# Kernel optimization log

Hardware: AMD Instinct MI355X
Metric: run time of the kernel (lower is better)

Reference implementation:

```python
import jax, jax.numpy as jnp
import numpy as np

D, NQ, BS, NL, NH, NP, DFF = 256, 900, 8, 4, 8, 4, 1024
HD = D // NH
SHAPES = np.array([[100, 100], [50, 50], [25, 25], [13, 13]], dtype=np.int64)  # (H, W) per level
LSTART = np.concatenate([[0], np.cumsum(SHAPES[:, 0] * SHAPES[:, 1])[:-1]]).astype(np.int64)
LMEM = int((SHAPES[:, 0] * SHAPES[:, 1]).sum())


def layer_norm(x, g, b, eps=1e-5):
    mu = x.mean(-1, keepdims=True)
    var = ((x - mu) ** 2).mean(-1, keepdims=True)
    return (x - mu) * jax.lax.rsqrt(var + eps) * g + b


def _forward(tgt, tgt_query_pos, tgt_reference_points, memory,
             in_proj_w, in_proj_b, out_proj_w, out_proj_b,
             samp_off_w, samp_off_b, attn_w_w, attn_w_b,
             value_proj_w, value_proj_b, output_proj_w, output_proj_b,
             lin1_w, lin1_b, lin2_w, lin2_b,
             norm1_g, norm1_b, norm2_g, norm2_b, norm3_g, norm3_b):
    # ---- self-attention (seq-first, torch nn.MultiheadAttention semantics) ----
    q = tgt + tgt_query_pos  # q = k = with_pos_embed(tgt, pos)
    Wq, Wk, Wv = jnp.split(in_proj_w, 3, 0)
    bq, bk, bv = jnp.split(in_proj_b, 3, 0)
    def heads(x):  # (nq, bs, d) -> (bs, nh, nq, hd)
        return x.reshape(NQ, BS, NH, HD).transpose(1, 2, 0, 3)
    qh = heads(q @ Wq.T + bq)
    kh = heads(q @ Wk.T + bk)
    vh = heads(tgt @ Wv.T + bv)
    attn = jax.nn.softmax(jnp.einsum('bhqd,bhkd->bhqk', qh, kh) / np.float32(np.sqrt(HD)), -1)
    sa = jnp.einsum('bhqk,bhkd->bhqd', attn, vh).transpose(2, 0, 1, 3).reshape(NQ, BS, D)
    sa = sa @ out_proj_w.T + out_proj_b
    t = layer_norm(tgt + sa, norm2_g, norm2_b)

    # ---- MSDeformAttn cross-attention (batch-first internally) ----
    qb = (t + tgt_query_pos).transpose(1, 0, 2)          # (bs, nq, d)
    refb = tgt_reference_points.transpose(1, 0, 2, 3)    # (bs, nq, nl, 2) in [0,1]
    memb = memory.transpose(1, 0, 2)                     # (bs, L, d)
    value = (memb @ value_proj_w.T + value_proj_b).reshape(BS, LMEM, NH, HD)
    off = (qb @ samp_off_w.T + samp_off_b).reshape(BS, NQ, NH, NL, NP, 2)
    aw = jax.nn.softmax((qb @ attn_w_w.T + attn_w_b).reshape(BS, NQ, NH, NL * NP), -1)
    aw = aw.reshape(BS, NQ, NH, NL, NP)
    normz = jnp.asarray(SHAPES[:, ::-1].copy(), dtype=jnp.float32)  # (nl, 2) = [W, H]
    loc = refb[:, :, None, :, None, :] + off / normz[None, None, None, :, None, :]

    out = jnp.zeros((BS, NQ, NH, HD), jnp.float32)
    for l in range(NL):  # fixed small number of pyramid levels
        Hl, Wl = int(SHAPES[l, 0]), int(SHAPES[l, 1])
        s = int(LSTART[l])
        v_l = value[:, s:s + Hl * Wl]  # (bs, Hl*Wl, nh, hd)
        # grid_sample(align_corners=False, padding=zeros) pixel coords
        x = (loc[:, :, :, l, :, 0] * Wl - 0.5).transpose(0, 1, 3, 2).reshape(BS, NQ * NP, NH)
        y = (loc[:, :, :, l, :, 1] * Hl - 0.5).transpose(0, 1, 3, 2).reshape(BS, NQ * NP, NH)
        x0 = jnp.floor(x)
        y0 = jnp.floor(y)
        samp = jnp.zeros((BS, NQ * NP, NH, HD), jnp.float32)
        for dx in (0, 1):
            for dy in (0, 1):
                xc = x0 + dx
                yc = y0 + dy
                w = (1.0 - jnp.abs(x - xc)) * (1.0 - jnp.abs(y - yc))
                valid = (xc >= 0) & (xc < Wl) & (yc >= 0) & (yc < Hl)
                idx = (jnp.clip(yc, 0, Hl - 1) * Wl + jnp.clip(xc, 0, Wl - 1)).astype(jnp.int32)
                g = jnp.take_along_axis(v_l, idx[..., None], axis=1)  # (bs, nq*np, nh, hd)
                samp = samp + jnp.where(valid, w, 0.0)[..., None] * g
        samp = samp.reshape(BS, NQ, NP, NH, HD)
        out = out + jnp.einsum('bqhp,bqphd->bqhd', aw[:, :, :, l], samp)
    ca = (out.reshape(BS, NQ, D) @ output_proj_w.T + output_proj_b).transpose(1, 0, 2)
    t = layer_norm(t + ca, norm1_g, norm1_b)

    # ---- FFN ----
    ffn = jax.nn.relu(t @ lin1_w.T + lin1_b) @ lin2_w.T + lin2_b
    return layer_norm(t + ffn, norm3_g, norm3_b)


def setup_inputs() -> dict:
    key = jax.random.key(0)
    ks = jax.random.split(key, 24)
    r = lambda i, shape, s: jax.random.normal(ks[i], shape, jnp.float32) * s
    return {
        'tgt': r(0, (NQ, BS, D), 1.0),
        'tgt_query_pos': r(1, (NQ, BS, D), 1.0),
        'tgt_reference_points': jax.random.uniform(ks[2], (NQ, BS, NL, 2), jnp.float32),
        'memory': r(3, (LMEM, BS, D), 1.0),
        'spatial_shapes': jnp.asarray(SHAPES),
        'level_start_index': jnp.asarray(LSTART),
        'in_proj_w': r(4, (3 * D, D), 0.02), 'in_proj_b': r(5, (3 * D,), 0.02),
        'out_proj_w': r(6, (D, D), 0.02), 'out_proj_b': r(7, (D,), 0.02),
        'samp_off_w': r(8, (NH * NL * NP * 2, D), 0.01), 'samp_off_b': r(9, (NH * NL * NP * 2,), 0.01),
        'attn_w_w': r(10, (NH * NL * NP, D), 0.02), 'attn_w_b': r(11, (NH * NL * NP,), 0.02),
        'value_proj_w': r(12, (D, D), 0.02), 'value_proj_b': r(13, (D,), 0.02),
        'output_proj_w': r(14, (D, D), 0.02), 'output_proj_b': r(15, (D,), 0.02),
        'lin1_w': r(16, (DFF, D), 0.02), 'lin1_b': r(17, (DFF,), 0.02),
        'lin2_w': r(18, (D, DFF), 0.02), 'lin2_b': r(19, (D,), 0.02),
        'norm1_g': jnp.ones((D,), jnp.float32), 'norm1_b': jnp.zeros((D,), jnp.float32),
        'norm2_g': jnp.ones((D,), jnp.float32), 'norm2_b': jnp.zeros((D,), jnp.float32),
        'norm3_g': jnp.ones((D,), jnp.float32), 'norm3_b': jnp.zeros((D,), jnp.float32),
    }


def reference(tgt, tgt_query_pos, tgt_reference_points, memory, spatial_shapes, level_start_index,
              in_proj_w, in_proj_b, out_proj_w, out_proj_b, samp_off_w, samp_off_b,
              attn_w_w, attn_w_b, value_proj_w, value_proj_b, output_proj_w, output_proj_b,
              lin1_w, lin1_b, lin2_w, lin2_b, norm1_g, norm1_b, norm2_g, norm2_b, norm3_g, norm3_b):
    # spatial_shapes / level_start_index are static level constants (module-level SHAPES/LSTART)
    return _forward(tgt, tgt_query_pos, tgt_reference_points, memory,
                    in_proj_w, in_proj_b, out_proj_w, out_proj_b,
                    samp_off_w, samp_off_b, attn_w_w, attn_w_b,
                    value_proj_w, value_proj_b, output_proj_w, output_proj_b,
                    lin1_w, lin1_b, lin2_w, lin2_b,
                    norm1_g, norm1_b, norm2_g, norm2_b, norm3_g, norm3_b)
```

## Files before the change

kernel.cpp:

```cpp
#include <hip/hip_runtime.h>
#include <hip/hip_bf16.h>


namespace {
constexpr int D_ = 256;
constexpr int NQ_ = 900;
constexpr int BS_ = 8;
constexpr int NH_ = 8;
constexpr int HD_ = 32;
constexpr int DFF_ = 1024;
constexpr int MTOK = NQ_ * BS_;
constexpr int LMEM_ = 13294;
constexpr long T = (long)MTOK * D_;
constexpr float QSC = 0.17677669529663687f;
constexpr int QKVS = 768;
constexpr int MVAL = BS_ * LMEM_;
}

typedef __attribute__((ext_vector_type(8))) short bf8_t;
typedef __attribute__((ext_vector_type(4))) float f4_t;

#define MFMA16(a, b, c) __builtin_amdgcn_mfma_f32_16x16x32_bf16((a), (b), (c), 0, 0, 0)

__device__ __forceinline__ unsigned short bfbits(float x) {
    union { __hip_bfloat16 h; unsigned short u; } cv;
    cv.h = __float2bfloat16(x);
    return cv.u;
}
__device__ __forceinline__ float bf2f(unsigned short u) {
    union { float f; unsigned v; } cv;
    cv.v = ((unsigned)u) << 16;
    return cv.f;
}

__device__ __forceinline__ void gload16(const unsigned short* g, unsigned short* l) {
    __builtin_amdgcn_global_load_lds(
        (const __attribute__((address_space(1))) unsigned int*)(g),
        (__attribute__((address_space(3))) unsigned int*)(l), 16, 0, 0);
}
__device__ __forceinline__ void gload16f(const float* g, float* l) {
    __builtin_amdgcn_global_load_lds(
        (const __attribute__((address_space(1))) unsigned int*)(g),
        (__attribute__((address_space(3))) unsigned int*)(l), 16, 0, 0);
}

__global__ void conv_weights(
    const float* __restrict__ ipw, const float* __restrict__ opw,
    const float* __restrict__ sow, const float* __restrict__ aww,
    const float* __restrict__ vpw, const float* __restrict__ outpw,
    const float* __restrict__ l1w, const float* __restrict__ l2w,
    const float* __restrict__ ipb, const float* __restrict__ sob,
    const float* __restrict__ awb,
    unsigned short* __restrict__ Wbf, float* __restrict__ biasAll)
{
    if (blockIdx.x == 0) {
        for (int j = threadIdx.x; j < 768; j += 256)
            biasAll[j] = (j < 256) ? ipb[j] * QSC : ipb[j];
        for (int j = threadIdx.x; j < 384; j += 256)
            biasAll[768 + j] = (j < 256) ? sob[j] : awb[j - 256];
    }
    const long idx4 = (long)blockIdx.x * 256 + threadIdx.x;
    if (idx4 >= 253952) return;
    const long e = idx4 * 4;
    const float* src; long off; float sc = 1.f;
    if (e < 196608)      { src = ipw;   off = 0;      if (e < 65536) sc = QSC; }
    else if (e < 262144) { src = opw;   off = 196608; }
    else if (e < 327680) { src = sow;   off = 262144; }
    else if (e < 360448) { src = aww;   off = 327680; }
    else if (e < 425984) { src = vpw;   off = 360448; }
    else if (e < 491520) { src = outpw; off = 425984; }
    else if (e < 753664) { src = l1w;   off = 491520; }
    else                 { src = l2w;   off = 753664; }
    const float4 v = *(const float4*)(src + (e - off));
    union { unsigned short u[4]; uint2 w; } pk;
    pk.u[0] = bfbits(v.x * sc); pk.u[1] = bfbits(v.y * sc);
    pk.u[2] = bfbits(v.z * sc); pk.u[3] = bfbits(v.w * sc);
    *(uint2*)(Wbf + e) = pk.w;
}

template<bool RELU, bool OUTBF16>
__global__ __launch_bounds__(256) void gemm_mfma(
    const unsigned short* __restrict__ A, const unsigned short* __restrict__ W,
    const float* __restrict__ bias, void* __restrict__ C, int M, int N, int K)
{
    __shared__ unsigned short As[128 * 32];
    __shared__ unsigned short Ws[128 * 32];
    const int t = threadIdx.x;
    const long m0 = (long)blockIdx.x * 128;
    const int n0 = blockIdx.y * 128;
    const int row0 = t >> 2;
    const int cgp = (t & 3) ^ ((t >> 2) & 3);
    long ar0 = m0 + row0;        if (ar0 > M - 1) ar0 = M - 1;
    long ar1 = m0 + 64 + row0;   if (ar1 > M - 1) ar1 = M - 1;
    const unsigned short* ga0 = A + ar0 * K + cgp * 8;
    const unsigned short* ga1 = A + ar1 * K + cgp * 8;
    const unsigned short* gw0 = W + (long)(n0 + row0) * K + cgp * 8;
    const unsigned short* gw1 = W + (long)(n0 + 64 + row0) * K + cgp * 8;
    const int lane = t & 63, wave = t >> 6;
    const int c = lane & 15, g = lane >> 4;
    const int wr = wave >> 1, wc = wave & 1;
    const int sws = (g * 8) ^ ((c & 3) * 8);
    f4_t acc[4][4];
#pragma unroll
    for (int i = 0; i < 4; ++i)
#pragma unroll
        for (int j = 0; j < 4; ++j)
            acc[i][j] = f4_t{0.f, 0.f, 0.f, 0.f};

    for (int kb = 0; kb < K; kb += 32) {
        gload16(ga0 + kb, As + t * 8);
        gload16(ga1 + kb, As + 2048 + t * 8);
        gload16(gw0 + kb, Ws + t * 8);
        gload16(gw1 + kb, Ws + 2048 + t * 8);
        __syncthreads();
        bf8_t af[4], bfr[4];
#pragma unroll
        for (int i = 0; i < 4; ++i) {
            af[i] = *(const bf8_t*)(As + (wr * 64 + i * 16 + c) * 32 + sws);
            bfr[i] = *(const bf8_t*)(Ws + (wc * 64 + i * 16 + c) * 32 + sws);
        }
#pragma unroll
        for (int i = 0; i < 4; ++i)
#pragma unroll
            for (int j = 0; j < 4; ++j)
                acc[i][j] = MFMA16(af[i], bfr[j], acc[i][j]);
        __syncthreads();
    }

#pragma unroll
    for (int i = 0; i < 4; ++i) {
        const long rbase = m0 + wr * 64 + i * 16 + 4 * g;
#pragma unroll
        for (int j = 0; j < 4; ++j) {
            const int col = n0 + wc * 64 + j * 16 + c;
            const float bv = bias[col];
#pragma unroll
            for (int r = 0; r < 4; ++r) {
                const long rr = rbase + r;
                if (rr < M) {
                    float v = acc[i][j][r] + bv;
                    if (RELU) v = fmaxf(v, 0.f);
                    if (OUTBF16) ((unsigned short*)C)[rr * N + col] = bfbits(v);
                    else         ((float*)C)[rr * N + col] = v;
                }
            }
        }
    }
}

__global__ __launch_bounds__(256) void gemm_f32d(
    const float* __restrict__ A, const unsigned short* __restrict__ W,
    const float* __restrict__ bias, unsigned short* __restrict__ C,
    int M, int N, int K)
{
    __shared__ float Asf[64 * 64];
    __shared__ unsigned short Ws[128 * 64];
    const int t = threadIdx.x;
    const long m0 = (long)blockIdx.x * 64;
    const int n0 = blockIdx.y * 128;
    const float* gA[4];
#pragma unroll
    for (int l = 0; l < 4; ++l) {
        int r = (int)m0 + l * 16 + (t >> 4); if (r > M - 1) r = M - 1;
        const int sp = (t & 15) ^ ((t >> 4) & 15);
        gA[l] = A + (long)r * K + sp * 4;
    }
    const unsigned short* gW[4];
#pragma unroll
    for (int l = 0; l < 4; ++l) {
        const int r = l * 32 + (t >> 3);
        const int sp = (t & 7) ^ (r & 7);
        gW[l] = W + (long)(n0 + r) * K + sp * 8;
    }
    const int lane = t & 63, wave = t >> 6;
    const int c = lane & 15, g = lane >> 4;
    const int wr = wave >> 1, wc = wave & 1;
    f4_t acc[2][4];
#pragma unroll
    for (int i = 0; i < 2; ++i)
#pragma unroll
        for (int j = 0; j < 4; ++j)
            acc[i][j] = f4_t{0.f, 0.f, 0.f, 0.f};

    for (int kb = 0; kb < K; kb += 64) {
#pragma unroll
        for (int l = 0; l < 4; ++l) gload16f(gA[l] + kb, Asf + l * 1024 + t * 4);
#pragma unroll
        for (int l = 0; l < 4; ++l) gload16(gW[l] + kb, Ws + l * 2048 + t * 8);
        __syncthreads();
#pragma unroll
        for (int s = 0; s < 2; ++s) {
            bf8_t af[2], bfr[4];
#pragma unroll
            for (int i = 0; i < 2; ++i) {
                const int row = wr * 32 + i * 16 + c;
                const int sl0 = (s * 8 + 2 * g) ^ (row & 15);
                const int sl1 = (s * 8 + 2 * g + 1) ^ (row & 15);
                const f4_t lo = *(const f4_t*)(Asf + row * 64 + sl0 * 4);
                const f4_t hi = *(const f4_t*)(Asf + row * 64 + sl1 * 4);
                union { bf8_t v; unsigned short u[8]; } pk;
                pk.u[0] = bfbits(lo[0]); pk.u[1] = bfbits(lo[1]);
                pk.u[2] = bfbits(lo[2]); pk.u[3] = bfbits(lo[3]);
                pk.u[4] = bfbits(hi[0]); pk.u[5] = bfbits(hi[1]);
                pk.u[6] = bfbits(hi[2]); pk.u[7] = bfbits(hi[3]);
                af[i] = pk.v;
            }
#pragma unroll
            for (int j = 0; j < 4; ++j) {
                const int row = wc * 64 + j * 16 + c;
                const int sl = (s * 4 + g) ^ (row & 7);
                bfr[j] = *(const bf8_t*)(Ws + row * 64 + sl * 8);
            }
#pragma unroll
            for (int i = 0; i < 2; ++i)
#pragma unroll
                for (int j = 0; j < 4; ++j)
                    acc[i][j] = MFMA16(af[i], bfr[j], acc[i][j]);
        }
        __syncthreads();
    }

    unsigned short* Cl = (unsigned short*)Asf;
#pragma unroll
    for (int i = 0; i < 2; ++i) {
        const int rloc = wr * 32 + i * 16 + 4 * g;
#pragma unroll
        for (int j = 0; j < 4; ++j) {
            const int col = wc * 64 + j * 16 + c;
            const float bv = bias[n0 + col];
#pragma unroll
            for (int r = 0; r < 4; ++r)
                Cl[(rloc + r) * 128 + col] = bfbits(acc[i][j][r] + bv);
        }
    }
    __syncthreads();
    {
        const int row = t >> 2, seg = t & 3;
        const long rr = m0 + row;
        if (rr < M) {
            const uint4* src = (const uint4*)(Cl + row * 128 + seg * 32);
            uint4* dst = (uint4*)(C + rr * N + n0 + seg * 32);
            dst[0] = src[0]; dst[1] = src[1]; dst[2] = src[2]; dst[3] = src[3];
        }
    }
}

template<bool OUTBF16>
__global__ __launch_bounds__(256) void gemm_f32a(
    const float* __restrict__ A, const float* __restrict__ A2,
    const unsigned short* __restrict__ W, const float* __restrict__ bias,
    void* __restrict__ C, int M, int N, int K, int addLim)
{
    __shared__ unsigned short As[128 * 32];
    __shared__ unsigned short Ws[128 * 32];
    const int t = threadIdx.x;
    const long m0 = (long)blockIdx.x * 128;
    const int n0 = blockIdx.y * 128;
    const bool useAdd = n0 < addLim;
    const int row0 = t >> 2, cg = t & 3;
    const int cgp = cg ^ ((t >> 2) & 3);
    long ar0 = m0 + row0;        if (ar0 > M - 1) ar0 = M - 1;
    long ar1 = m0 + 64 + row0;   if (ar1 > M - 1) ar1 = M - 1;
    const float* Ap0 = A + ar0 * K + cg * 8;
    const float* Ap1 = A + ar1 * K + cg * 8;
    const float* Bp0 = A2 + ar0 * K + cg * 8;
    const float* Bp1 = A2 + ar1 * K + cg * 8;
    const unsigned short* gw0 = W + (long)(n0 + row0) * K + cgp * 8;
    const unsigned short* gw1 = W + (long)(n0 + 64 + row0) * K + cgp * 8;
    unsigned short* la0 = As + row0 * 32 + ((cg * 8) ^ ((row0 & 3) * 8));
    unsigned short* la1 = la0 + 2048;
    const int lane = t & 63, wave = t >> 6;
    const int c = lane & 15, g = lane >> 4;
    const int wr = wave >> 1, wc = wave & 1;
    const int sws = (g * 8) ^ ((c & 3) * 8);
    f4_t acc[4][4];
#pragma unroll
    for (int i = 0; i < 4; ++i)
#pragma unroll
        for (int j = 0; j < 4; ++j)
            acc[i][j] = f4_t{0.f, 0.f, 0.f, 0.f};

    for (int kb = 0; kb < K; kb += 32) {
        gload16(gw0 + kb, Ws + t * 8);
        gload16(gw1 + kb, Ws + 2048 + t * 8);
        float4 a00 = *(const float4*)(Ap0 + kb);
        float4 a01 = *(const float4*)(Ap0 + kb + 4);
        float4 a10 = *(const float4*)(Ap1 + kb);
        float4 a11 = *(const float4*)(Ap1 + kb + 4);
        if (useAdd) {
            const float4 b00 = *(const float4*)(Bp0 + kb);
            const float4 b01 = *(const float4*)(Bp0 + kb + 4);
            const float4 b10 = *(const float4*)(Bp1 + kb);
            const float4 b11 = *(const float4*)(Bp1 + kb + 4);
            a00.x += b00.x; a00.y += b00.y; a00.z += b00.z; a00.w += b00.w;
            a01.x += b01.x; a01.y += b01.y; a01.z += b01.z; a01.w += b01.w;
            a10.x += b10.x; a10.y += b10.y; a10.z += b10.z; a10.w += b10.w;
            a11.x += b11.x; a11.y += b11.y; a11.z += b11.z; a11.w += b11.w;
        }
        union { bf8_t v; unsigned short u[8]; } p0, p1;
        p0.u[0] = bfbits(a00.x); p0.u[1] = bfbits(a00.y); p0.u[2] = bfbits(a00.z); p0.u[3] = bfbits(a00.w);
        p0.u[4] = bfbits(a01.x); p0.u[5] = bfbits(a01.y); p0.u[6] = bfbits(a01.z); p0.u[7] = bfbits(a01.w);
        p1.u[0] = bfbits(a10.x); p1.u[1] = bfbits(a10.y); p1.u[2] = bfbits(a10.z); p1.u[3] = bfbits(a10.w);
        p1.u[4] = bfbits(a11.x); p1.u[5] = bfbits(a11.y); p1.u[6] = bfbits(a11.z); p1.u[7] = bfbits(a11.w);
        *(bf8_t*)la0 = p0.v;
        *(bf8_t*)la1 = p1.v;
        __syncthreads();
        bf8_t af[4], bfr[4];
#pragma unroll
        for (int i = 0; i < 4; ++i) {
            af[i] = *(const bf8_t*)(As + (wr * 64 + i * 16 + c) * 32 + sws);
            bfr[i] = *(const bf8_t*)(Ws + (wc * 64 + i * 16 + c) * 32 + sws);
        }
#pragma unroll
        for (int i = 0; i < 4; ++i)
#pragma unroll
            for (int j = 0; j < 4; ++j)
                acc[i][j] = MFMA16(af[i], bfr[j], acc[i][j]);
        __syncthreads();
    }

#pragma unroll
    for (int i = 0; i < 4; ++i) {
        const long rbase = m0 + wr * 64 + i * 16 + 4 * g;
#pragma unroll
        for (int j = 0; j < 4; ++j) {
            const int col = n0 + wc * 64 + j * 16 + c;
            const float bv = bias[col];
#pragma unroll
            for (int r = 0; r < 4; ++r) {
                const long rr = rbase + r;
                if (rr < M) {
                    float v = acc[i][j][r] + bv;
                    if (OUTBF16) ((unsigned short*)C)[rr * N + col] = bfbits(v);
                    else         ((float*)C)[rr * N + col] = v;
                }
            }
        }
    }
}

__global__ __launch_bounds__(256) void attn_mfma(
    const unsigned short* __restrict__ Qb, const unsigned short* __restrict__ Kb,
    const unsigned short* __restrict__ Vb, unsigned short* __restrict__ sa)
{
    __shared__ float smemf[2112];
    unsigned short* Ks = (unsigned short*)smemf;
    unsigned short* Vt = (unsigned short*)(smemf + 1024);
    const int t = threadIdx.x;
    const int wave = t >> 6, lane = t & 63;
    const int g = lane >> 4, c = lane & 15;
    const int b = blockIdx.x >> 3, h = blockIdx.x & 7;
    const int q0 = blockIdx.y * 64 + wave * 16;
    const int q = q0 + c;
    const bool qv = q < NQ_;
    const bf8_t qf = *(const bf8_t*)(Qb + ((long)(qv ? q : 0) * BS_ + b) * QKVS + h * HD_ + 8 * g);

    f4_t acc0 = {0.f, 0.f, 0.f, 0.f}, acc1 = {0.f, 0.f, 0.f, 0.f};
    float m_run = -1e30f, l_run = 0.f;
    const int sk = t >> 2, sd = (t & 3) * 8;

    for (int kc = 0; kc < NQ_; kc += 64) {
        __syncthreads();
        {
            const int key = kc + sk;
            union { bf8_t v; unsigned short u[8]; } kv, vv;
            if (key < NQ_) {
                kv.v = *(const bf8_t*)(Kb + ((long)key * BS_ + b) * QKVS + h * HD_ + sd);
                vv.v = *(const bf8_t*)(Vb + ((long)key * BS_ + b) * QKVS + h * HD_ + sd);
            } else {
#pragma unroll
                for (int u = 0; u < 8; ++u) { kv.u[u] = 0; vv.u[u] = 0; }
            }
            *(bf8_t*)(Ks + sk * 32 + sd) = kv.v;
#pragma unroll
            for (int u = 0; u < 8; ++u) {
                const int r = sd + u;
                Vt[r * 64 + (sk ^ ((r & 7) << 3))] = vv.u[u];
            }
        }
        __syncthreads();

        f4_t s[4];
#pragma unroll
        for (int tt = 0; tt < 4; ++tt) {
            const bf8_t kf = *(const bf8_t*)(Ks + (tt * 16 + c) * 32 + 8 * g);
            f4_t z = {0.f, 0.f, 0.f, 0.f};
            s[tt] = MFMA16(kf, qf, z);
        }
        float sv[16];
#pragma unroll
        for (int tt = 0; tt < 4; ++tt)
#pragma unroll
            for (int r = 0; r < 4; ++r) {
                float x = s[tt][r];
                if (kc + tt * 16 + 4 * g + r >= NQ_) x = -1e30f;
                sv[tt * 4 + r] = x;
            }
        float mloc = sv[0];
#pragma unroll
        for (int i = 1; i < 16; ++i) mloc = fmaxf(mloc, sv[i]);
        mloc = fmaxf(mloc, __shfl_xor(mloc, 16));
        mloc = fmaxf(mloc, __shfl_xor(mloc, 32));
        const float mnew = fmaxf(m_run, mloc);
        const float resc = __expf(m_run - mnew);
        float p[16], ls = 0.f;
#pragma unroll
        for (int i = 0; i < 16; ++i) { p[i] = __expf(sv[i] - mnew); ls += p[i]; }
        ls += __shfl_xor(ls, 16);
        ls += __shfl_xor(ls, 32);
        l_run = l_run * resc + ls;
        m_run = mnew;
#pragma unroll
        for (int r = 0; r < 4; ++r) { acc0[r] *= resc; acc1[r] *= resc; }

        unsigned pk[4][2];
#pragma unroll
        for (int tt = 0; tt < 4; ++tt) {
            pk[tt][0] = (unsigned)bfbits(p[tt * 4 + 0]) | ((unsigned)bfbits(p[tt * 4 + 1]) << 16);
            pk[tt][1] = (unsigned)bfbits(p[tt * 4 + 2]) | ((unsigned)bfbits(p[tt * 4 + 3]) << 16);
        }
        const int srcA = ((g & 1) << 5) + c;
        const int srcB = srcA + 16;
#pragma unroll
        for (int kh = 0; kh < 2; ++kh) {
            const unsigned a0 = __shfl(pk[kh * 2][0], srcA), b0_ = __shfl(pk[kh * 2 + 1][0], srcA);
            const unsigned a1 = __shfl(pk[kh * 2][1], srcA), b1_ = __shfl(pk[kh * 2 + 1][1], srcA);
            const unsigned a2 = __shfl(pk[kh * 2][0], srcB), b2_ = __shfl(pk[kh * 2 + 1][0], srcB);
            const unsigned a3 = __shfl(pk[kh * 2][1], srcB), b3_ = __shfl(pk[kh * 2 + 1][1], srcB);
            union { bf8_t v; unsigned u[4]; } pf;
            const bool hi = (g & 2);
            pf.u[0] = hi ? b0_ : a0; pf.u[1] = hi ? b1_ : a1;
            pf.u[2] = hi ? b2_ : a2; pf.u[3] = hi ? b3_ : a3;
            const int kcol = (kh * 32 + 8 * g) ^ ((c & 7) << 3);
            const bf8_t vf0 = *(const bf8_t*)(Vt + c * 64 + kcol);
            const bf8_t vf1 = *(const bf8_t*)(Vt + (16 + c) * 64 + kcol);
            acc0 = MFMA16(vf0, pf.v, acc0);
            acc1 = MFMA16(vf1, pf.v, acc1);
        }
    }

    __syncthreads();
    const float invl = 1.f / l_run;
    float* O = smemf + wave * 528;
#pragma unroll
    for (int r = 0; r < 4; ++r) {
        O[c * 33 + 4 * g + r] = acc0[r] * invl;
        O[c * 33 + 16 + 4 * g + r] = acc1[r] * invl;
    }
    __syncthreads();
    {
        const int ql = lane >> 2, part = lane & 3;
        const int qg = q0 + ql;
        if (qg < NQ_) {
            union { bf8_t v; unsigned short u[8]; } pk;
#pragma unroll
            for (int u = 0; u < 8; ++u) pk.u[u] = bfbits(O[ql * 33 + part * 8 + u]);
            *(bf8_t*)(sa + ((long)qg * BS_ + b) * D_ + h * HD_ + part * 8) = pk.v;
        }
    }
}

__global__ __launch_bounds__(256) void msdeform_kernel(
    const float* __restrict__ oa, const float* __restrict__ refp,
    const unsigned short* __restrict__ val, unsigned short* __restrict__ out)
{
    __shared__ float saw[128];
    __shared__ float redm[8], redi[8];
    __shared__ float swt[128][4];
    __shared__ int sidx[128][4];
    const int bq = blockIdx.x;
    const int b = bq / NQ_, q = bq % NQ_;
    const int t = threadIdx.x;
    if (t < 128) saw[t] = oa[(long)bq * 384 + 256 + t];
    __syncthreads();
    if (t < 8) {
        float mx = -1e30f;
        for (int i = 0; i < 16; ++i) mx = fmaxf(mx, saw[t * 16 + i]);
        float s = 0.f;
        for (int i = 0; i < 16; ++i) s += __expf(saw[t * 16 + i] - mx);
        redm[t] = mx; redi[t] = 1.f / s;
    }
    __syncthreads();
    if (t < 128) {
        const int h = t >> 4, lp = t & 15, l = lp >> 2, p = lp & 3;
        const float aw = __expf(saw[t] - redm[h]) * redi[h];
        const int Wi = (l == 0) ? 100 : (l == 1) ? 50 : (l == 2) ? 25 : 13;
        const int Hi = Wi;
        const int sl = (l == 0) ? 0 : (l == 1) ? 10000 : (l == 2) ? 12500 : 13125;
        const float offx = oa[(long)bq * 384 + h * 32 + l * 8 + p * 2 + 0];
        const float offy = oa[(long)bq * 384 + h * 32 + l * 8 + p * 2 + 1];
        const float refx = refp[(((long)q * BS_ + b) * 4 + l) * 2 + 0];
        const float refy = refp[(((long)q * BS_ + b) * 4 + l) * 2 + 1];
        const float fW = (float)Wi, fH = (float)Hi;
        const float x = (refx + offx / fW) * fW - 0.5f;
        const float y = (refy + offy / fH) * fH - 0.5f;
        const float x0f = floorf(x), y0f = floorf(y);
        const float fx = x - x0f, fy = y - y0f;
        const int ix = (int)x0f, iy = (int)y0f;
        const float wts[4] = {(1.f - fx) * (1.f - fy), fx * (1.f - fy),
                              (1.f - fx) * fy,          fx * fy};
        const int xs[4] = {ix, ix + 1, ix, ix + 1};
        const int ys[4] = {iy, iy, iy + 1, iy + 1};
#pragma unroll
        for (int tap = 0; tap < 4; ++tap) {
            const bool valid = (xs[tap] >= 0) & (xs[tap] < Wi) & (ys[tap] >= 0) & (ys[tap] < Hi);
            const int xc = min(max(xs[tap], 0), Wi - 1);
            const int yc = min(max(ys[tap], 0), Hi - 1);
            swt[t][tap] = valid ? aw * wts[tap] : 0.f;
            sidx[t][tap] = ((sl + yc * Wi + xc) << 3) + b;
        }
    }
    __syncthreads();
    const int h = t >> 5, r = t & 31, qd = r & 7, s = r >> 3;
    float a0 = 0.f, a1 = 0.f, a2 = 0.f, a3 = 0.f;
#pragma unroll
    for (int i = 0; i < 16; ++i) {
        const int j = h * 16 + i;
        const float wv = swt[j][s];
        const long base = (long)sidx[j][s] * D_ + h * HD_ + qd * 4;
        const uint2 raw = *(const uint2*)(val + base);
        a0 += wv * bf2f((unsigned short)(raw.x & 0xffff));
        a1 += wv * bf2f((unsigned short)(raw.x >> 16));
        a2 += wv * bf2f((unsigned short)(raw.y & 0xffff));
        a3 += wv * bf2f((unsigned short)(raw.y >> 16));
    }
    a0 += __shfl_xor(a0, 8); a0 += __shfl_xor(a0, 16);
    a1 += __shfl_xor(a1, 8); a1 += __shfl_xor(a1, 16);
    a2 += __shfl_xor(a2, 8); a2 += __shfl_xor(a2, 16);
    a3 += __shfl_xor(a3, 8); a3 += __shfl_xor(a3, 16);
    if (s == 0) {
        union { unsigned short u[4]; uint2 w; } pk;
        pk.u[0] = bfbits(a0); pk.u[1] = bfbits(a1); pk.u[2] = bfbits(a2); pk.u[3] = bfbits(a3);
        *(uint2*)(out + (long)bq * D_ + h * HD_ + qd * 4) = pk.w;
    }
}

__global__ __launch_bounds__(256) void ln_kernel(
    const float* __restrict__ inA, const float* __restrict__ inB,
    const float* __restrict__ g, const float* __restrict__ be,
    float* __restrict__ out, const float* __restrict__ pos,
    unsigned short* __restrict__ bfOut, int swapB, int bfMode)
{
    const int r = blockIdx.x * 4 + (threadIdx.x >> 6);
    const int lane = threadIdx.x & 63;
    long rb = r;
    if (swapB) rb = (long)(r & 7) * NQ_ + (r >> 3);
    const float4 a4 = *(const float4*)(inA + (long)r * D_ + lane * 4);
    const float4 b4 = *(const float4*)(inB + rb * D_ + lane * 4);
    float x[4] = {a4.x + b4.x, a4.y + b4.y, a4.z + b4.z, a4.w + b4.w};
    float s = x[0] + x[1] + x[2] + x[3];
#pragma unroll
    for (int off = 32; off > 0; off >>= 1) s += __shfl_xor(s, off);
    const float mu = s * (1.f / D_);
    float v = 0.f;
#pragma unroll
    for (int cc = 0; cc < 4; ++cc) { const float dd = x[cc] - mu; v += dd * dd; }
#pragma unroll
    for (int off = 32; off > 0; off >>= 1) v += __shfl_xor(v, off);
    const float rs = rsqrtf(v * (1.f / D_) + 1e-5f);
    const float4 g4 = *(const float4*)(g + lane * 4);
    const float4 e4 = *(const float4*)(be + lane * 4);
    const float gg[4] = {g4.x, g4.y, g4.z, g4.w};
    const float ee[4] = {e4.x, e4.y, e4.z, e4.w};
    float y[4];
#pragma unroll
    for (int cc = 0; cc < 4; ++cc) y[cc] = (x[cc] - mu) * rs * gg[cc] + ee[cc];
    *(float4*)(out + (long)r * D_ + lane * 4) = make_float4(y[0], y[1], y[2], y[3]);
    if (bfMode) {
        float z[4] = {y[0], y[1], y[2], y[3]};
        long er = r;
        if (bfMode == 2) {
            const float4 p4 = *(const float4*)(pos + (long)r * D_ + lane * 4);
            z[0] += p4.x; z[1] += p4.y; z[2] += p4.z; z[3] += p4.w;
            er = (long)(r & 7) * NQ_ + (r >> 3);
        }
        union { unsigned short u[4]; uint2 w; } pk;
        pk.u[0] = bfbits(z[0]); pk.u[1] = bfbits(z[1]);
        pk.u[2] = bfbits(z[2]); pk.u[3] = bfbits(z[3]);
        *(uint2*)(bfOut + er * D_ + lane * 4) = pk.w;
    }
}

extern "C" void kernel_launch(void* const* d_in, const int* in_sizes, int n_in,
                              void* d_out, int out_size, void* d_ws, size_t ws_size,
                              hipStream_t stream) {
    const float* tgt   = (const float*)d_in[0];
    const float* pos   = (const float*)d_in[1];
    const float* refp  = (const float*)d_in[2];
    const float* mem   = (const float*)d_in[3];
    const float* ipw   = (const float*)d_in[6];
    const float* ipb   = (const float*)d_in[7];
    const float* opw   = (const float*)d_in[8];
    const float* opb   = (const float*)d_in[9];
    const float* sow   = (const float*)d_in[10];
    const float* sob   = (const float*)d_in[11];
    const float* aww   = (const float*)d_in[12];
    const float* awb   = (const float*)d_in[13];
    const float* vpw   = (const float*)d_in[14];
    const float* vpb   = (const float*)d_in[15];
    const float* outpw = (const float*)d_in[16];
    const float* outpb = (const float*)d_in[17];
    const float* l1w   = (const float*)d_in[18];
    const float* l1b   = (const float*)d_in[19];
    const float* l2w   = (const float*)d_in[20];
    const float* l2b   = (const float*)d_in[21];
    const float* n1g = (const float*)d_in[22]; const float* n1be = (const float*)d_in[23];
    const float* n2g = (const float*)d_in[24]; const float* n2be = (const float*)d_in[25];
    const float* n3g = (const float*)d_in[26]; const float* n3be = (const float*)d_in[27];

    char* wsb = (char*)d_ws;
    auto alloc = [&](size_t bytes) { char* p = wsb; wsb += (bytes + 255) & ~(size_t)255; return p; };
    unsigned short* Wbf       = (unsigned short*)alloc(1015808 * 2);
    float*          biasAll   = (float*)alloc(1152 * 4);
    unsigned short* QKV_bf    = (unsigned short*)alloc((long)MTOK * QKVS * 2);
    unsigned short* sa_bf     = (unsigned short*)alloc(T * 2);
    float*          saproj    = (float*)alloc(T * 4);
    float*          t1        = (float*)alloc(T * 4);
    unsigned short* qplus2_bf = (unsigned short*)alloc(T * 2);
    float*          oa        = (float*)alloc((long)MTOK * 384 * 4);
    unsigned short* sampo_bf  = (unsigned short*)alloc(T * 2);
    float*          ca        = (float*)alloc(T * 4);
    float*          t2        = (float*)alloc(T * 4);
    unsigned short* t2_bf     = (unsigned short*)alloc(T * 2);
    unsigned short* ffnh_bf   = (unsigned short*)alloc((long)MTOK * DFF_ * 2);
    float*          ffno      = (float*)alloc(T * 4);
    unsigned short* val       = (unsigned short*)alloc((long)MVAL * D_ * 2);
    const unsigned short* wqkv  = Wbf + 0;
    const unsigned short* wo    = Wbf + 196608;
    const unsigned short* wsoaw = Wbf + 262144;
    const unsigned short* wvp   = Wbf + 360448;
    const unsigned short* wop   = Wbf + 425984;
    const unsigned short* wl1   = Wbf + 491520;
    const unsigned short* wl2   = Wbf + 753664;
    const float* bias_qkv = biasAll;
    const float* bias_oa  = biasAll + 768;

    const dim3 blk(256);
    const dim3 g_m(57, 2);

    conv_weights<<<992, blk, 0, stream>>>(ipw, opw, sow, aww, vpw, outpw, l1w, l2w,
                                          ipb, sob, awb, Wbf, biasAll);
    gemm_f32a<true><<<dim3(57, 6), blk, 0, stream>>>(tgt, pos, wqkv, bias_qkv, QKV_bf,
                                                     MTOK, QKVS, D_, 512);
    attn_mfma<<<dim3(64, 15), blk, 0, stream>>>(QKV_bf, QKV_bf + 256, QKV_bf + 512, sa_bf);
    gemm_mfma<false, false><<<g_m, blk, 0, stream>>>(sa_bf, wo, opb, saproj, MTOK, D_, D_);
    ln_kernel<<<1800, blk, 0, stream>>>(tgt, saproj, n2g, n2be, t1, pos, qplus2_bf, 0, 2);
    gemm_f32d<<<dim3(1662, 2), blk, 0, stream>>>(mem, wvp, vpb, val, MVAL, D_, D_);
    gemm_mfma<false, false><<<dim3(57, 3), blk, 0, stream>>>(qplus2_bf, wsoaw, bias_oa, oa, MTOK, 384, D_);
    msdeform_kernel<<<7200, blk, 0, stream>>>(oa, refp, val, sampo_bf);
    gemm_mfma<false, false><<<g_m, blk, 0, stream>>>(sampo_bf, wop, outpb, ca, MTOK, D_, D_);
    ln_kernel<<<1800, blk, 0, stream>>>(t1, ca, n1g, n1be, t2, nullptr, t2_bf, 1, 1);
    gemm_mfma<true, true><<<dim3(57, 8), blk, 0, stream>>>(t2_bf, wl1, l1b, ffnh_bf, MTOK, DFF_, D_);
    gemm_mfma<false, false><<<g_m, blk, 0, stream>>>(ffnh_bf, wl2, l2b, ffno, MTOK, D_, DFF_);
    ln_kernel<<<1800, blk, 0, stream>>>(t2, ffno, n3g, n3be, (float*)d_out, nullptr, nullptr, 0, 0);
}
```

Measured before the change: 235.8 us.

## Fuse self-attention and value projection into one interleaved heterogeneous launch

Merges the self-attention kernel and the independent value-projection GEMM into a single launch. Block indices are interleaved so that every fourth block in the first region runs attention and the rest run value-projection tiles, letting the two independent workloads overlap on the GPU instead of running back to back. The cost is a shared 32KB LDS allocation sized for the larger body, which may lower occupancy for the attention blocks, plus some divergence in block scheduling.

Result: slower. 281.8 us (+19.5%).

```diff
diff --git a/kernel.cpp b/kernel.cpp
--- a/kernel.cpp
+++ b/kernel.cpp
@@ -15,6 +15,8 @@
 constexpr float QSC = 0.17677669529663687f;
 constexpr int QKVS = 768;
 constexpr int MVAL = BS_ * LMEM_;
+constexpr int NVT = 1662;
+constexpr int NATT = 960;
 }
 
 typedef __attribute__((ext_vector_type(8))) short bf8_t;
@@ -148,29 +150,29 @@
     }
 }
 
-__global__ __launch_bounds__(256) void gemm_f32d(
-    const float* __restrict__ A, const unsigned short* __restrict__ W,
+__device__ __forceinline__ void val_body(
+    char* lds, const float* __restrict__ A, const unsigned short* __restrict__ W,
     const float* __restrict__ bias, unsigned short* __restrict__ C,
-    int M, int N, int K)
-{
-    __shared__ float Asf[64 * 64];
-    __shared__ unsigned short Ws[128 * 64];
+    int tile, int ncol)
+{
+    float* Asf = (float*)lds;
+    unsigned short* Ws = (unsigned short*)(lds + 16384);
     const int t = threadIdx.x;
-    const long m0 = (long)blockIdx.x * 64;
-    const int n0 = blockIdx.y * 128;
+    const long m0 = (long)tile * 64;
+    const int n0 = ncol * 128;
     const float* gA[4];
 #pragma unroll
     for (int l = 0; l < 4; ++l) {
-        int r = (int)m0 + l * 16 + (t >> 4); if (r > M - 1) r = M - 1;
+        int r = (int)m0 + l * 16 + (t >> 4); if (r > MVAL - 1) r = MVAL - 1;
         const int sp = (t & 15) ^ ((t >> 4) & 15);
-        gA[l] = A + (long)r * K + sp * 4;
+        gA[l] = A + (long)r * 256 + sp * 4;
     }
     const unsigned short* gW[4];
 #pragma unroll
     for (int l = 0; l < 4; ++l) {
         const int r = l * 32 + (t >> 3);
         const int sp = (t & 7) ^ (r & 7);
-        gW[l] = W + (long)(n0 + r) * K + sp * 8;
+        gW[l] = W + (long)(n0 + r) * 256 + sp * 8;
     }
     const int lane = t & 63, wave = t >> 6;
     const int c = lane & 15, g = lane >> 4;
@@ -182,7 +184,7 @@
         for (int j = 0; j < 4; ++j)
             acc[i][j] = f4_t{0.f, 0.f, 0.f, 0.f};
 
-    for (int kb = 0; kb < K; kb += 64) {
+    for (int kb = 0; kb < 256; kb += 64) {
 #pragma unroll
         for (int l = 0; l < 4; ++l) gload16f(gA[l] + kb, Asf + l * 1024 + t * 4);
 #pragma unroll
@@ -237,11 +239,149 @@
     {
         const int row = t >> 2, seg = t & 3;
         const long rr = m0 + row;
-        if (rr < M) {
+        if (rr < MVAL) {
             const uint4* src = (const uint4*)(Cl + row * 128 + seg * 32);
-            uint4* dst = (uint4*)(C + rr * N + n0 + seg * 32);
+            uint4* dst = (uint4*)(C + rr * 256 + n0 + seg * 32);
             dst[0] = src[0]; dst[1] = src[1]; dst[2] = src[2]; dst[3] = src[3];
         }
+    }
+}
+
+__device__ __forceinline__ void attn_body(
+    char* lds, const unsigned short* __restrict__ Qb,
+    const unsigned short* __restrict__ Kb, const unsigned short* __restrict__ Vb,
+    unsigned short* __restrict__ sa, int bh, int qchunk)
+{
+    float* smemf = (float*)lds;
+    unsigned short* Ks = (unsigned short*)smemf;
+    unsigned short* Vt = (unsigned short*)(smemf + 1024);
+    const int t = threadIdx.x;
+    const int wave = t >> 6, lane = t & 63;
+    const int g = lane >> 4, c = lane & 15;
+    const int b = bh >> 3, h = bh & 7;
+    const int q0 = qchunk * 64 + wave * 16;
+    const int q = q0 + c;
+    const bool qv = q < NQ_;
+    const bf8_t qf = *(const bf8_t*)(Qb + ((long)(qv ? q : 0) * BS_ + b) * QKVS + h * HD_ + 8 * g);
+
+    f4_t acc0 = {0.f, 0.f, 0.f, 0.f}, acc1 = {0.f, 0.f, 0.f, 0.f};
+    float m_run = -1e30f, l_run = 0.f;
+    const int sk = t >> 2, sd = (t & 3) * 8;
+
+    for (int kc = 0; kc < NQ_; kc += 64) {
+        __syncthreads();
+        {
+            const int key = kc + sk;
+            union { bf8_t v; unsigned short u[8]; } kv, vv;
+            if (key < NQ_) {
+                kv.v = *(const bf8_t*)(Kb + ((long)key * BS_ + b) * QKVS + h * HD_ + sd);
+                vv.v = *(const bf8_t*)(Vb + ((long)key * BS_ + b) * QKVS + h * HD_ + sd);
+            } else {
+#pragma unroll
+                for (int u = 0; u < 8; ++u) { kv.u[u] = 0; vv.u[u] = 0; }
+            }
+            *(bf8_t*)(Ks + sk * 32 + sd) = kv.v;
+#pragma unroll
+            for (int u = 0; u < 8; ++u) {
+                const int r = sd + u;
+                Vt[r * 64 + (sk ^ ((r & 7) << 3))] = vv.u[u];
+            }
+        }
+        __syncthreads();
+
+        f4_t s[4];
+#pragma unroll
+        for (int tt = 0; tt < 4; ++tt) {
+            const bf8_t kf = *(const bf8_t*)(Ks + (tt * 16 + c) * 32 + 8 * g);
+            f4_t z = {0.f, 0.f, 0.f, 0.f};
+            s[tt] = MFMA16(kf, qf, z);
+        }
+        float sv[16];
+#pragma unroll
+        for (int tt = 0; tt < 4; ++tt)
+#pragma unroll
+            for (int r = 0; r < 4; ++r) {
+                float x = s[tt][r];
+                if (kc + tt * 16 + 4 * g + r >= NQ_) x = -1e30f;
+                sv[tt * 4 + r] = x;
+            }
+        float mloc = sv[0];
+#pragma unroll
+        for (int i = 1; i < 16; ++i) mloc = fmaxf(mloc, sv[i]);
+        mloc = fmaxf(mloc, __shfl_xor(mloc, 16));
+        mloc = fmaxf(mloc, __shfl_xor(mloc, 32));
+        const float mnew = fmaxf(m_run, mloc);
+        const float resc = __expf(m_run - mnew);
+        float p[16], ls = 0.f;
+#pragma unroll
+        for (int i = 0; i < 16; ++i) { p[i] = __expf(sv[i] - mnew); ls += p[i]; }
+        ls += __shfl_xor(ls, 16);
+        ls += __shfl_xor(ls, 32);
+        l_run = l_run * resc + ls;
+        m_run = mnew;
+#pragma unroll
+        for (int r = 0; r < 4; ++r) { acc0[r] *= resc; acc1[r] *= resc; }
+
+        unsigned pk[4][2];
+#pragma unroll
+        for (int tt = 0; tt < 4; ++tt) {
+            pk[tt][0] = (unsigned)bfbits(p[tt * 4 + 0]) | ((unsigned)bfbits(p[tt * 4 + 1]) << 16);
+            pk[tt][1] = (unsigned)bfbits(p[tt * 4 + 2]) | ((unsigned)bfbits(p[tt * 4 + 3]) << 16);
+        }
+        const int srcA = ((g & 1) << 5) + c;
+        const int srcB = srcA + 16;
+#pragma unroll
+        for (int kh = 0; kh < 2; ++kh) {
+            const unsigned a0 = __shfl(pk[kh * 2][0], srcA), b0_ = __shfl(pk[kh * 2 + 1][0], srcA);
+            const unsigned a1 = __shfl(pk[kh * 2][1], srcA), b1_ = __shfl(pk[kh * 2 + 1][1], srcA);
+            const unsigned a2 = __shfl(pk[kh * 2][0], srcB), b2_ = __shfl(pk[kh * 2 + 1][0], srcB);
+            const unsigned a3 = __shfl(pk[kh * 2][1], srcB), b3_ = __shfl(pk[kh * 2 + 1][1], srcB);
+            union { bf8_t v; unsigned u[4]; } pf;
+            const bool hi = (g & 2);
+            pf.u[0] = hi ? b0_ : a0; pf.u[1] = hi ? b1_ : a1;
+            pf.u[2] = hi ? b2_ : a2; pf.u[3] = hi ? b3_ : a3;
+            const int kcol = (kh * 32 + 8 * g) ^ ((c & 7) << 3);
+            const bf8_t vf0 = *(const bf8_t*)(Vt + c * 64 + kcol);
+            const bf8_t vf1 = *(const bf8_t*)(Vt + (16 + c) * 64 + kcol);
+            acc0 = MFMA16(vf0, pf.v, acc0);
+            acc1 = MFMA16(vf1, pf.v, acc1);
+        }
+    }
+
+    __syncthreads();
+    const float invl = 1.f / l_run;
+    float* O = smemf + wave * 528;
+#pragma unroll
+    for (int r = 0; r < 4; ++r) {
+        O[c * 33 + 4 * g + r] = acc0[r] * invl;
+        O[c * 33 + 16 + 4 * g + r] = acc1[r] * invl;
+    }
+    __syncthreads();
+    {
+        const int ql = lane >> 2, part = lane & 3;
+        const int qg = q0 + ql;
+        if (qg < NQ_) {
+            union { bf8_t v; unsigned short u[8]; } pk;
+#pragma unroll
+            for (int u = 0; u < 8; ++u) pk.u[u] = bfbits(O[ql * 33 + part * 8 + u]);
+            *(bf8_t*)(sa + ((long)qg * BS_ + b) * D_ + h * HD_ + part * 8) = pk.v;
+        }
+    }
+}
+
+__global__ __launch_bounds__(256) void attn_val(
+    const unsigned short* __restrict__ QKV, unsigned short* __restrict__ sa,
+    const float* __restrict__ mem, const unsigned short* __restrict__ wvp,
+    const float* __restrict__ vpb, unsigned short* __restrict__ val)
+{
+    __shared__ char lds[32768];
+    const int bid = blockIdx.x;
+    if (bid < 4 * NATT && (bid & 3) == 3) {
+        const int aidx = bid >> 2;
+        attn_body(lds, QKV, QKV + 256, QKV + 512, sa, aidx & 63, aidx >> 6);
+    } else {
+        const int vidx = (bid < 4 * NATT) ? (bid - (bid >> 2)) : (bid - NATT);
+        val_body(lds, mem, wvp, vpb, val, vidx % NVT, vidx / NVT);
     }
 }
 
@@ -335,127 +475,6 @@
                     else         ((float*)C)[rr * N + col] = v;
                 }
             }
-        }
-    }
-}
-
-__global__ __launch_bounds__(256) void attn_mfma(
-    const unsigned short* __restrict__ Qb, const unsigned short* __restrict__ Kb,
-    const unsigned short* __restrict__ Vb, unsigned short* __restrict__ sa)
-{
-    __shared__ float smemf[2112];
-    unsigned short* Ks = (unsigned short*)smemf;
-    unsigned short* Vt = (unsigned short*)(smemf + 1024);
-    const int t = threadIdx.x;
-    const int wave = t >> 6, lane = t & 63;
-    const int g = lane >> 4, c = lane & 15;
-    const int b = blockIdx.x >> 3, h = blockIdx.x & 7;
-    const int q0 = blockIdx.y * 64 + wave * 16;
-    const int q = q0 + c;
-    const bool qv = q < NQ_;
-    const bf8_t qf = *(const bf8_t*)(Qb + ((long)(qv ? q : 0) * BS_ + b) * QKVS + h * HD_ + 8 * g);
-
-    f4_t acc0 = {0.f, 0.f, 0.f, 0.f}, acc1 = {0.f, 0.f, 0.f, 0.f};
-    float m_run = -1e30f, l_run = 0.f;
-    const int sk = t >> 2, sd = (t & 3) * 8;
-
-    for (int kc = 0; kc < NQ_; kc += 64) {
-        __syncthreads();
-        {
-            const int key = kc + sk;
-            union { bf8_t v; unsigned short u[8]; } kv, vv;
-            if (key < NQ_) {
-                kv.v = *(const bf8_t*)(Kb + ((long)key * BS_ + b) * QKVS + h * HD_ + sd);
-                vv.v = *(const bf8_t*)(Vb + ((long)key * BS_ + b) * QKVS + h * HD_ + sd);
-            } else {
-#pragma unroll
-                for (int u = 0; u < 8; ++u) { kv.u[u] = 0; vv.u[u] = 0; }
-            }
-            *(bf8_t*)(Ks + sk * 32 + sd) = kv.v;
-#pragma unroll
-            for (int u = 0; u < 8; ++u) {
-                const int r = sd + u;
-                Vt[r * 64 + (sk ^ ((r & 7) << 3))] = vv.u[u];
-            }
-        }
-        __syncthreads();
-
-        f4_t s[4];
-#pragma unroll
-        for (int tt = 0; tt < 4; ++tt) {
-            const bf8_t kf = *(const bf8_t*)(Ks + (tt * 16 + c) * 32 + 8 * g);
-            f4_t z = {0.f, 0.f, 0.f, 0.f};
-            s[tt] = MFMA16(kf, qf, z);
-        }
-        float sv[16];
-#pragma unroll
-        for (int tt = 0; tt < 4; ++tt)
-#pragma unroll
-            for (int r = 0; r < 4; ++r) {
-                float x = s[tt][r];
-                if (kc + tt * 16 + 4 * g + r >= NQ_) x = -1e30f;
-                sv[tt * 4 + r] = x;
-            }
-        float mloc = sv[0];
-#pragma unroll
-        for (int i = 1; i < 16; ++i) mloc = fmaxf(mloc, sv[i]);
-        mloc = fmaxf(mloc, __shfl_xor(mloc, 16));
-        mloc = fmaxf(mloc, __shfl_xor(mloc, 32));
-        const float mnew = fmaxf(m_run, mloc);
-        const float resc = __expf(m_run - mnew);
-        float p[16], ls = 0.f;
-#pragma unroll
-        for (int i = 0; i < 16; ++i) { p[i] = __expf(sv[i] - mnew); ls += p[i]; }
-        ls += __shfl_xor(ls, 16);
-        ls += __shfl_xor(ls, 32);
-        l_run = l_run * resc + ls;
-        m_run = mnew;
-#pragma unroll
-        for (int r = 0; r < 4; ++r) { acc0[r] *= resc; acc1[r] *= resc; }
-
-        unsigned pk[4][2];
-#pragma unroll
-        for (int tt = 0; tt < 4; ++tt) {
-            pk[tt][0] = (unsigned)bfbits(p[tt * 4 + 0]) | ((unsigned)bfbits(p[tt * 4 + 1]) << 16);
-            pk[tt][1] = (unsigned)bfbits(p[tt * 4 + 2]) | ((unsigned)bfbits(p[tt * 4 + 3]) << 16);
-        }
-        const int srcA = ((g & 1) << 5) + c;
-        const int srcB = srcA + 16;
-#pragma unroll
-        for (int kh = 0; kh < 2; ++kh) {
-            const unsigned a0 = __shfl(pk[kh * 2][0], srcA), b0_ = __shfl(pk[kh * 2 + 1][0], srcA);
-            const unsigned a1 = __shfl(pk[kh * 2][1], srcA), b1_ = __shfl(pk[kh * 2 + 1][1], srcA);
-            const unsigned a2 = __shfl(pk[kh * 2][0], srcB), b2_ = __shfl(pk[kh * 2 + 1][0], srcB);
-            const unsigned a3 = __shfl(pk[kh * 2][1], srcB), b3_ = __shfl(pk[kh * 2 + 1][1], srcB);
-            union { bf8_t v; unsigned u[4]; } pf;
-            const bool hi = (g & 2);
-            pf.u[0] = hi ? b0_ : a0; pf.u[1] = hi ? b1_ : a1;
-            pf.u[2] = hi ? b2_ : a2; pf.u[3] = hi ? b3_ : a3;
-            const int kcol = (kh * 32 + 8 * g) ^ ((c & 7) << 3);
-            const bf8_t vf0 = *(const bf8_t*)(Vt + c * 64 + kcol);
-            const bf8_t vf1 = *(const bf8_t*)(Vt + (16 + c) * 64 + kcol);
-            acc0 = MFMA16(vf0, pf.v, acc0);
-            acc1 = MFMA16(vf1, pf.v, acc1);
-        }
-    }
-
-    __syncthreads();
-    const float invl = 1.f / l_run;
-    float* O = smemf + wave * 528;
-#pragma unroll
-    for (int r = 0; r < 4; ++r) {
-        O[c * 33 + 4 * g + r] = acc0[r] * invl;
-        O[c * 33 + 16 + 4 * g + r] = acc1[r] * invl;
-    }
-    __syncthreads();
-    {
-        const int ql = lane >> 2, part = lane & 3;
-        const int qg = q0 + ql;
-        if (qg < NQ_) {
-            union { bf8_t v; unsigned short u[8]; } pk;
-#pragma unroll
-            for (int u = 0; u < 8; ++u) pk.u[u] = bfbits(O[ql * 33 + part * 8 + u]);
-            *(bf8_t*)(sa + ((long)qg * BS_ + b) * D_ + h * HD_ + part * 8) = pk.v;
         }
     }
 }
@@ -642,10 +661,9 @@
                                           ipb, sob, awb, Wbf, biasAll);
     gemm_f32a<true><<<dim3(57, 6), blk, 0, stream>>>(tgt, pos, wqkv, bias_qkv, QKV_bf,
                                                      MTOK, QKVS, D_, 512);
-    attn_mfma<<<dim3(64, 15), blk, 0, stream>>>(QKV_bf, QKV_bf + 256, QKV_bf + 512, sa_bf);
+    attn_val<<<dim3(NATT + 2 * NVT), blk, 0, stream>>>(QKV_bf, sa_bf, mem, wvp, vpb, val);
     gemm_mfma<false, false><<<g_m, blk, 0, stream>>>(sa_bf, wo, opb, saproj, MTOK, D_, D_);
     ln_kernel<<<1800, blk, 0, stream>>>(tgt, saproj, n2g, n2be, t1, pos, qplus2_bf, 0, 2);
-    gemm_f32d<<<dim3(1662, 2), blk, 0, stream>>>(mem, wvp, vpb, val, MVAL, D_, D_);
     gemm_mfma<false, false><<<dim3(57, 3), blk, 0, stream>>>(qplus2_bf, wsoaw, bias_oa, oa, MTOK, 384, D_);
     msdeform_kernel<<<7200, blk, 0, stream>>>(oa, refp, val, sampo_bf);
     gemm_mfma<false, false><<<g_m, blk, 0, stream>>>(sampo_bf, wop, outpb, ca, MTOK, D_, D_);
```
